# Kernel optimization log

Measured on AMD Instinct MI355X. Metric: run time of the kernel, lower is better.

## Reference

```python
import jax, jax.numpy as jnp
import numpy as np

DIM = 1024
HEADS = 16
HEAD_DIM = DIM // HEADS
LAYERS = 8
HIDDEN = 4 * DIM
VOCAB = 266
MAX_POS = 32768
B = 4
L = 2048
SCALE = HEAD_DIM ** -0.5
EPS = 1e-5


def layer_norm(x, g, b):
    m = jnp.mean(x, axis=-1, keepdims=True)
    v = jnp.mean(jnp.square(x - m), axis=-1, keepdims=True)
    return (x - m) * jax.lax.rsqrt(v + EPS) * g + b


def setup_inputs() -> dict:
    key = jax.random.key(0)
    ks = jax.random.split(key, 16)
    s = 0.02
    return {
        "tokens": jax.random.randint(ks[0], (B, L), 0, VOCAB),
        "tok_emb": jax.random.normal(ks[1], (VOCAB, DIM), jnp.float32) * s,
        "pos_emb": jax.random.normal(ks[2], (MAX_POS, DIM), jnp.float32) * s,
        "ln1_g": jnp.ones((LAYERS, DIM), jnp.float32),
        "ln1_b": jnp.zeros((LAYERS, DIM), jnp.float32),
        "q_w": jax.random.normal(ks[3], (LAYERS, DIM, DIM), jnp.float32) * s,
        "k_w": jax.random.normal(ks[4], (LAYERS, DIM, DIM), jnp.float32) * s,
        "v_w": jax.random.normal(ks[5], (LAYERS, DIM, DIM), jnp.float32) * s,
        "o_w": jax.random.normal(ks[6], (LAYERS, DIM, DIM), jnp.float32) * s,
        "ln2_g": jnp.ones((LAYERS, DIM), jnp.float32),
        "ln2_b": jnp.zeros((LAYERS, DIM), jnp.float32),
        "w1_w": jax.random.normal(ks[7], (LAYERS, HIDDEN, DIM), jnp.float32) * s,
        "wg_w": jax.random.normal(ks[8], (LAYERS, HIDDEN, DIM), jnp.float32) * s,
        "w2_w": jax.random.normal(ks[9], (LAYERS, DIM, HIDDEN), jnp.float32) * s,
        "lnf_g": jnp.ones((DIM,), jnp.float32),
        "lnf_b": jnp.zeros((DIM,), jnp.float32),
        "lm_w": jax.random.normal(ks[10], (VOCAB, DIM), jnp.float32) * s,
    }


def reference(tokens, tok_emb, pos_emb, ln1_g, ln1_b, q_w, k_w, v_w, o_w,
              ln2_g, ln2_b, w1_w, wg_w, w2_w, lnf_g, lnf_b, lm_w):
    Bv, Lv = tokens.shape
    x = tok_emb[tokens] + pos_emb[jnp.arange(Lv)][None, :, :]  # [B,L,D]
    # strictly-upper-triangular causal mask (True = masked)
    rows = jnp.arange(Lv)
    mask = rows[None, :] > rows[:, None]  # [L,L], col > row
    pos_bias = jnp.arange(Lv, dtype=x.dtype) * 0.01  # [L]
    neg_inf = jnp.array(-jnp.inf, dtype=x.dtype)

    for i in range(LAYERS):
        h = layer_norm(x, ln1_g[i], ln1_b[i])
        q = jnp.einsum('bld,ed->ble', h, q_w[i]).reshape(Bv, Lv, HEADS, HEAD_DIM).transpose(0, 2, 1, 3)
        k = jnp.einsum('bld,ed->ble', h, k_w[i]).reshape(Bv, Lv, HEADS, HEAD_DIM).transpose(0, 2, 1, 3)
        v = jnp.einsum('bld,ed->ble', h, v_w[i]).reshape(Bv, Lv, HEADS, HEAD_DIM).transpose(0, 2, 1, 3)
        attn = jnp.einsum('bhqd,bhkd->bhqk', q, k) * SCALE
        attn = jnp.where(mask[None, None, :, :], neg_inf, attn)
        attn = attn + pos_bias[None, None, None, :]
        attn = jax.nn.softmax(attn, axis=-1)
        out = jnp.einsum('bhqk,bhkd->bhqd', attn, v).transpose(0, 2, 1, 3).reshape(Bv, Lv, DIM)
        attn_out = jnp.einsum('bld,ed->ble', out, o_w[i])
        x = x + attn_out
        h2 = layer_norm(x, ln2_g[i], ln2_b[i])
        ff = jnp.einsum('blh,dh->bld', jax.nn.silu(jnp.einsum('bld,hd->blh', h2, w1_w[i])) * jnp.einsum('bld,hd->blh', h2, wg_w[i]), w2_w[i])
        x = x + ff

    last = layer_norm(x[:, -1, :], lnf_g, lnf_b)  # [B, D]
    return jnp.einsum('bd,vd->bv', last, lm_w)  # [B, VOCAB]
```

## Files before the change

kernel.cpp:

```cpp
#include <hip/hip_runtime.h>
#include <hip/hip_bf16.h>
#include <math.h>

#define DIMD 1024
#define HEADS 16
#define HD 64
#define LAYERS 8
#define HIDDEN 4096
#define VOCAB 266
#define NB 4
#define SEQ 2048
#define ROWS (NB*SEQ)
#define LOG2E 1.4426950408889634f
#define QSCALE (0.125f * LOG2E)
#define BIAS2 (0.01f * LOG2E)
#define THR2 8.0f

typedef float f32x4 __attribute__((ext_vector_type(4)));
typedef __bf16 bf16x8 __attribute__((ext_vector_type(8)));
typedef __bf16 bf16x4 __attribute__((ext_vector_type(4)));

__device__ __forceinline__ f32x4 mfma16(bf16x8 a, bf16x8 b, f32x4 c) {
    return __builtin_amdgcn_mfma_f32_16x16x32_bf16(a, b, c, 0, 0, 0);
}

__device__ __forceinline__ void gload16(const __bf16* g, __bf16* l) {
    __builtin_amdgcn_global_load_lds(
        (const __attribute__((address_space(1))) void*)g,
        (__attribute__((address_space(3))) void*)l, 16, 0, 0);
}

__global__ void embed_kernel(const int* __restrict__ tok, const float* __restrict__ te,
                             const float* __restrict__ pe, float* __restrict__ x) {
    int row = blockIdx.x;
    int t = tok[row];
    int l = row & (SEQ - 1);
    int c = threadIdx.x;
    f32x4 tv = *(const f32x4*)(te + (size_t)t * DIMD + c * 4);
    f32x4 pv = *(const f32x4*)(pe + (size_t)l * DIMD + c * 4);
    *(f32x4*)(x + (size_t)row * DIMD + c * 4) = tv + pv;
}

__global__ void cvt_kernel(const float* q, const float* k, const float* v, const float* o,
                           const float* w1, const float* wg, const float* w2,
                           __bf16* __restrict__ dst) {
    const size_t MM = 1024 * 1024;
    const float* src; size_t n; size_t off; int ilv = 0;
    switch (blockIdx.y) {
        case 0: src = q;  n = MM;     off = 0;       break;
        case 1: src = k;  n = MM;     off = MM;      break;
        case 2: src = v;  n = MM;     off = 2 * MM;  break;
        case 3: src = o;  n = MM;     off = 3 * MM;  break;
        case 4: src = w1; n = 4 * MM; off = 4 * MM;  ilv = 1; break;
        case 5: src = wg; n = 4 * MM; off = 4 * MM;  ilv = 2; break;
        default: src = w2; n = 4 * MM; off = 12 * MM; break;
    }
    size_t stride = (size_t)gridDim.x * blockDim.x * 8;
    for (size_t i = ((size_t)blockIdx.x * blockDim.x + threadIdx.x) * 8; i < n; i += stride) {
        f32x4 a = *(const f32x4*)(src + i);
        f32x4 b = *(const f32x4*)(src + i + 4);
        bf16x8 ov;
        ov[0] = (__bf16)a[0]; ov[1] = (__bf16)a[1]; ov[2] = (__bf16)a[2]; ov[3] = (__bf16)a[3];
        ov[4] = (__bf16)b[0]; ov[5] = (__bf16)b[1]; ov[6] = (__bf16)b[2]; ov[7] = (__bf16)b[3];
        size_t di;
        if (ilv) {
            size_t row = i >> 10, col = i & 1023;
            di = off + (((row << 1) | (ilv - 1)) << 10) + col;
        } else {
            di = off + i;
        }
        *(bf16x8*)(dst + di) = ov;
    }
}

template<bool F32OUT>
__global__ void ln_kernel(const float* __restrict__ xin, size_t row_stride,
                          const float* __restrict__ g, const float* __restrict__ bb,
                          void* __restrict__ out) {
    int row = blockIdx.x;
    int c = threadIdx.x;
    const float* xr = xin + (size_t)row * row_stride;
    f32x4 v = *(const f32x4*)(xr + c * 4);
    float s = v[0] + v[1] + v[2] + v[3];
    float s2 = v[0]*v[0] + v[1]*v[1] + v[2]*v[2] + v[3]*v[3];
    #pragma unroll
    for (int o = 32; o; o >>= 1) { s += __shfl_xor(s, o); s2 += __shfl_xor(s2, o); }
    __shared__ float red[8];
    int w = c >> 6, lane = c & 63;
    if (lane == 0) { red[w] = s; red[4 + w] = s2; }
    __syncthreads();
    s = red[0] + red[1] + red[2] + red[3];
    s2 = red[4] + red[5] + red[6] + red[7];
    float mean = s * (1.f / DIMD);
    float var = s2 * (1.f / DIMD) - mean * mean;
    float rstd = rsqrtf(var + 1e-5f);
    f32x4 gv = *(const f32x4*)(g + c * 4);
    f32x4 bv = *(const f32x4*)(bb + c * 4);
    f32x4 o4;
    #pragma unroll
    for (int j = 0; j < 4; ++j) o4[j] = (v[j] - mean) * rstd * gv[j] + bv[j];
    if (F32OUT) {
        *(f32x4*)((float*)out + (size_t)row * DIMD + c * 4) = o4;
    } else {
        bf16x4 hv;
        #pragma unroll
        for (int j = 0; j < 4; ++j) hv[j] = (__bf16)o4[j];
        *(bf16x4*)((__bf16*)out + (size_t)row * DIMD + c * 4) = hv;
    }
}

template<int EPI>
__global__ __launch_bounds__(256, 3)
void gemm_bt(const __bf16* __restrict__ A, const __bf16* __restrict__ W,
             int M, int N, int K,
             __bf16* bdst, float* fdst, float scale) {
    __shared__ __bf16 As[128 * 64];
    __shared__ __bf16 Bs[128 * 64];
    int tid = threadIdx.x;
    int lane = tid & 63, w = tid >> 6;
    int wm = w >> 1, wn = w & 1;
    int g16 = lane >> 4, l16 = lane & 15;
    int m0 = blockIdx.y * 128, n0 = blockIdx.x * 128;
    f32x4 acc[4][4] = {};
    int trow = tid >> 3;
    int cs8 = ((tid & 7) ^ (trow & 7)) * 8;
    const __bf16* ga = A + (size_t)(m0 + trow) * K + cs8;
    const __bf16* gb = W + (size_t)(n0 + trow) * K + cs8;
    int xsw = (l16 & 7) << 4;

    for (int k0 = 0; k0 < K; k0 += 64) {
        #pragma unroll
        for (int p = 0; p < 4; ++p) {
            gload16(ga + (size_t)(p * 32) * K + k0, As + (p * 256 + w * 64) * 8);
            gload16(gb + (size_t)(p * 32) * K + k0, Bs + (p * 256 + w * 64) * 8);
        }
        __syncthreads();
        #pragma unroll
        for (int kk = 0; kk < 2; ++kk) {
            bf16x8 af[4], bfv[4];
            #pragma unroll
            for (int f = 0; f < 4; ++f) {
                int ar = wm * 64 + f * 16 + l16;
                int br = wn * 64 + f * 16 + l16;
                af[f]  = *(const bf16x8*)((const char*)As + ((ar * 128 + kk * 64 + g16 * 16) ^ xsw));
                bfv[f] = *(const bf16x8*)((const char*)Bs + ((br * 128 + kk * 64 + g16 * 16) ^ xsw));
            }
            #pragma unroll
            for (int fm = 0; fm < 4; ++fm)
                #pragma unroll
                for (int fn = 0; fn < 4; ++fn)
                    acc[fm][fn] = mfma16(af[fm], bfv[fn], acc[fm][fn]);
        }
        __syncthreads();
    }

    #pragma unroll
    for (int fm = 0; fm < 4; ++fm) {
        int rbase = m0 + wm * 64 + fm * 16 + g16 * 4;
        #pragma unroll
        for (int fn = 0; fn < 4; ++fn) {
            int col = n0 + wn * 64 + fn * 16 + l16;
            if (EPI == 2) {
                #pragma unroll
                for (int j = 0; j < 4; ++j) {
                    size_t idx = (size_t)(rbase + j) * N + col;
                    fdst[idx] += acc[fm][fn][j];
                }
            }
        }
    }
}

template<int EPI>
__global__ __launch_bounds__(512, 2)
void gemm_8ph(const __bf16* __restrict__ A, const __bf16* __restrict__ W,
              int M, int N, int K, __bf16* __restrict__ bdst, float scale) {
    __shared__ __bf16 As[2][2][128 * 64];
    __shared__ __bf16 Bs[2][2][128 * 64];
    int tid = threadIdx.x;
    int lane = tid & 63, wid = tid >> 6;
    int wm = wid >> 2, wn = wid & 3;
    int g16 = lane >> 4, l16 = lane & 15;
    int m0 = blockIdx.y * 256, n0 = blockIdx.x * 256;

    int sr = tid >> 3, ch = tid & 7;
    int cs8 = (ch ^ (sr & 7)) * 8;
    int xsw = (l16 & 7) << 4;

    const __bf16* gA = A + (size_t)(m0 + sr) * K + cs8;
    const __bf16* gB = W + (size_t)(n0 + sr) * K + cs8;

    auto stA = [&](int buf, int half, int kt) {
        const __bf16* g = gA + (size_t)(half * 128) * K + kt * 64;
        __bf16* l = &As[buf][half][sr * 64 + ch * 8];
        gload16(g, l);
        gload16(g + (size_t)64 * K, l + 64 * 64);
    };
    auto stB = [&](int buf, int half, int kt) {
        const __bf16* g = gB + (size_t)(half * 128) * K + kt * 64;
        __bf16* l = &Bs[buf][half][sr * 64 + ch * 8];
        gload16(g, l);
        gload16(g + (size_t)64 * K, l + 64 * 64);
    };

    f32x4 acc[8][4] = {};
    bf16x8 bfr[4][2];

    auto dsA = [&](int buf, int q, bf16x8 (&afr)[2][2]) {
        const char* base = (const char*)&As[buf][wm][0];
        #pragma unroll
        for (int dm = 0; dm < 2; ++dm)
            #pragma unroll
            for (int kk = 0; kk < 2; ++kk) {
                int row = (q * 2 + dm) * 16 + l16;
                afr[dm][kk] = *(const bf16x8*)(base + ((row * 128 + kk * 64 + g16 * 16) ^ xsw));
            }
    };
    auto dsB = [&](int buf) {
        const char* base = (const char*)&Bs[buf][wn >> 1][0];
        #pragma unroll
        for (int n = 0; n < 4; ++n)
            #pragma unroll
            for (int kk = 0; kk < 2; ++kk) {
                int row = (wn & 1) * 64 + n * 16 + l16;
                bfr[n][kk] = *(const bf16x8*)(base + ((row * 128 + kk * 64 + g16 * 16) ^ xsw));
            }
    };
    auto mm = [&](int q, bf16x8 (&afr)[2][2]) {
        #pragma unroll
        for (int dm = 0; dm < 2; ++dm)
            #pragma unroll
            for (int n = 0; n < 4; ++n)
                #pragma unroll
                for (int kk = 0; kk < 2; ++kk)
                    acc[q * 2 + dm][n] = mfma16(afr[dm][kk], bfr[n][kk], acc[q * 2 + dm][n]);
    };

#define PH(Q)                                                \
    __builtin_amdgcn_s_barrier();                            \
    asm volatile("s_waitcnt lgkmcnt(0)" ::: "memory");       \
    __builtin_amdgcn_s_setprio(1);                           \
    mm(Q, afr);                                              \
    __builtin_amdgcn_s_setprio(0);

    int NI = K >> 7;

    stA(0, 0, 0); stA(0, 1, 0); stB(0, 0, 0); stB(0, 1, 0);
    stB(1, 0, 1); stB(1, 1, 1);
    asm volatile("s_waitcnt vmcnt(4)" ::: "memory");
    __builtin_amdgcn_s_barrier();

    for (int it = 0; it < NI; ++it) {
        bool more = (it + 1 < NI);
        int o = 2 * it + 1, e2 = o + 1, o2 = o + 2;
        { bf16x8 afr[2][2]; dsA(0, 0, afr); dsB(0); stA(1, 0, o);    PH(0); }
        { bf16x8 afr[2][2]; dsA(0, 1, afr); stA(1, 1, o);            PH(1); }
        { bf16x8 afr[2][2]; dsA(0, 2, afr); if (more) stB(0, 0, e2); PH(2); }
        { bf16x8 afr[2][2]; dsA(0, 3, afr); if (more) stB(0, 1, e2);
          if (more) asm volatile("s_waitcnt vmcnt(4)" ::: "memory");
          else      asm volatile("s_waitcnt vmcnt(0)" ::: "memory");
          PH(3); }
        { bf16x8 afr[2][2]; dsA(1, 0, afr); dsB(1); if (more) stA(0, 0, e2); PH(0); }
        { bf16x8 afr[2][2]; dsA(1, 1, afr); if (more) stA(0, 1, e2); PH(1); }
        { bf16x8 afr[2][2]; dsA(1, 2, afr); if (more) stB(1, 0, o2); PH(2); }
        { bf16x8 afr[2][2]; dsA(1, 3, afr); if (more) stB(1, 1, o2);
          if (more) asm volatile("s_waitcnt vmcnt(4)" ::: "memory");
          PH(3); }
    }
#undef PH

    #pragma unroll
    for (int m = 0; m < 8; ++m) {
        int rbase = m0 + wm * 128 + m * 16 + g16 * 4;
        #pragma unroll
        for (int n = 0; n < 4; ++n) {
            int col = n0 + wn * 64 + n * 16 + l16;
            if (EPI == 5) {
                int which = col >> 10;
                int c = col & 1023;
                int hh = c >> 6, d = c & 63;
                if (which == 2) {
                    int b = rbase >> 11, l = rbase & 2047;
                    __bf16* vp = bdst + 2 * (size_t)ROWS * DIMD;
                    bf16x4 hv;
                    #pragma unroll
                    for (int j = 0; j < 4; ++j) hv[j] = (__bf16)acc[m][n][j];
                    *(bf16x4*)(vp + ((size_t)(b * HEADS + hh) * HD + d) * SEQ + l) = hv;
                } else {
                    float sc = (which == 0) ? scale : 1.f;
                    __bf16* base = bdst + (size_t)which * ROWS * DIMD;
                    #pragma unroll
                    for (int j = 0; j < 4; ++j) {
                        int row = rbase + j;
                        int b = row >> 11, l = row & 2047;
                        base[(((size_t)(b * HEADS + hh) * SEQ + l) << 6) + d] =
                            (__bf16)(acc[m][n][j] * sc);
                    }
                }
            } else if (EPI == 6) {
                #pragma unroll
                for (int j = 0; j < 4; ++j) {
                    float own = acc[m][n][j];
                    float other = __shfl_xor(own, 1);
                    if (!(l16 & 1)) {
                        float si = own / (1.f + __expf(-own));
                        bdst[(size_t)(rbase + j) * (N >> 1) + (col >> 1)] = (__bf16)(si * other);
                    }
                }
            }
        }
    }
}

__global__ __launch_bounds__(256, 2)
void attn_kernel(const __bf16* __restrict__ qt, const __bf16* __restrict__ kt,
                 const __bf16* __restrict__ vt, __bf16* __restrict__ ao) {
    int lin = blockIdx.x;
    int bxm = lin >> 6;
    int g = lin & 63;
    int hh = g & 15, b = g >> 4;
    int tid = threadIdx.x, lane = tid & 63, w = tid >> 6;
    int g16 = lane >> 4, l16 = lane & 15;

    __shared__ __bf16 Ks[2][64 * 64];
    __shared__ __bf16 Vs[2][64 * 64];
    __shared__ __bf16 Ps[4 * 32 * 72];
    __bf16* Pw = Ps + w * (32 * 72);

    const __bf16* qbase = qt + (size_t)(b * HEADS + hh) * SEQ * HD;
    const __bf16* kbase = kt + (size_t)(b * HEADS + hh) * SEQ * HD;
    const __bf16* vbase = vt + (size_t)(b * HEADS + hh) * HD * SEQ;

    int rr = lane >> 3;
    int cs8 = ((lane & 7) ^ rr) * 8;

    for (int s = 0; s < 2; ++s) {
        int qtile = (s == 0) ? (15 - bxm) : bxm;
        int qb = qtile * 128;
        int nt = (qb >> 6) + 2;

        bf16x8 qf[2][2];
        #pragma unroll
        for (int rb = 0; rb < 2; ++rb)
            #pragma unroll
            for (int kk = 0; kk < 2; ++kk)
                qf[rb][kk] = *(const bf16x8*)(qbase + (size_t)(qb + w * 32 + rb * 16 + l16) * HD + kk * 32 + g16 * 8);

        f32x4 accO[2][4] = {};
        float mrow[2][4], lrow[2][4];
        #pragma unroll
        for (int rb = 0; rb < 2; ++rb)
            #pragma unroll
            for (int j = 0; j < 4; ++j) { mrow[rb][j] = -1e30f; lrow[rb][j] = 0.f; }

        #pragma unroll
        for (int p = 0; p < 2; ++p) {
            int rbse = p * 32 + w * 8;
            gload16(kbase + (size_t)(rbse + rr) * HD + cs8, Ks[0] + rbse * 64);
            gload16(vbase + (size_t)(rbse + rr) * SEQ + cs8, Vs[0] + rbse * 64);
        }
        __syncthreads();

        for (int t = 0; t < nt; ++t) {
            int cur = t & 1;
            int kv0 = t << 6;

            if (t + 1 < nt) {
                int kv1 = kv0 + 64;
                #pragma unroll
                for (int p = 0; p < 2; ++p) {
                    int rbse = p * 32 + w * 8;
                    gload16(kbase + (size_t)(kv1 + rbse + rr) * HD + cs8, Ks[cur ^ 1] + rbse * 64);
                    gload16(vbase + (size_t)(rbse + rr) * SEQ + kv1 + cs8, Vs[cur ^ 1] + rbse * 64);
                }
            }

            f32x4 sacc[2][4] = {};
            __builtin_amdgcn_s_setprio(1);
            #pragma unroll
            for (int kk = 0; kk < 2; ++kk) {
                bf16x8 kf[4];
                #pragma unroll
                for (int nk = 0; nk < 4; ++nk) {
                    int key = nk * 16 + l16;
                    int bo = (key * 128 + (kk * 32 + g16 * 8) * 2) ^ ((key & 7) << 4);
                    kf[nk] = *(const bf16x8*)((const char*)Ks[cur] + bo);
                }
                #pragma unroll
                for (int rb = 0; rb < 2; ++rb)
                    #pragma unroll
                    for (int nk = 0; nk < 4; ++nk)
                        sacc[rb][nk] = mfma16(qf[rb][kk], kf[nk], sacc[rb][nk]);
            }
            __builtin_amdgcn_s_setprio(0);

            float mx8[2][4];
            #pragma unroll
            for (int rb = 0; rb < 2; ++rb) {
                #pragma unroll
                for (int j = 0; j < 4; ++j) {
                    int qrow = qb + w * 32 + rb * 16 + g16 * 4 + j;
                    float mx = -1e30f;
                    #pragma unroll
                    for (int nk = 0; nk < 4; ++nk) {
                        int key = kv0 + nk * 16 + l16;
                        float sc = sacc[rb][nk][j];
                        sc = (key <= qrow) ? (sc + BIAS2 * (float)key) : -1e30f;
                        sacc[rb][nk][j] = sc;
                        mx = fmaxf(mx, sc);
                    }
                    mx = fmaxf(mx, __shfl_xor(mx, 1));
                    mx = fmaxf(mx, __shfl_xor(mx, 2));
                    mx = fmaxf(mx, __shfl_xor(mx, 4));
                    mx = fmaxf(mx, __shfl_xor(mx, 8));
                    mx8[rb][j] = mx;
                }
            }

            bool ok = true;
            #pragma unroll
            for (int rb = 0; rb < 2; ++rb)
                #pragma unroll
                for (int j = 0; j < 4; ++j)
                    ok &= (mx8[rb][j] <= mrow[rb][j] + THR2);
            if (!__all(ok)) {
                #pragma unroll
                for (int rb = 0; rb < 2; ++rb) {
                    #pragma unroll
                    for (int j = 0; j < 4; ++j) {
                        float mnew = fmaxf(mrow[rb][j], mx8[rb][j]);
                        float rs = exp2f(mrow[rb][j] - mnew);
                        mrow[rb][j] = mnew;
                        lrow[rb][j] *= rs;
                        #pragma unroll
                        for (int nd = 0; nd < 4; ++nd) accO[rb][nd][j] *= rs;
                    }
                }
            }

            #pragma unroll
            for (int rb = 0; rb < 2; ++rb) {
                #pragma unroll
                for (int j = 0; j < 4; ++j) {
                    float m = mrow[rb][j];
                    float ps = 0.f;
                    #pragma unroll
                    for (int nk = 0; nk < 4; ++nk) {
                        float pp = exp2f(sacc[rb][nk][j] - m);
                        ps += pp;
                        Pw[(rb * 16 + g16 * 4 + j) * 72 + nk * 16 + l16] = (__bf16)pp;
                    }
                    lrow[rb][j] += ps;
                }
            }

            __builtin_amdgcn_s_setprio(1);
            #pragma unroll
            for (int kk = 0; kk < 2; ++kk) {
                bf16x8 pf[2];
                #pragma unroll
                for (int rb = 0; rb < 2; ++rb)
                    pf[rb] = *(const bf16x8*)(Pw + (rb * 16 + l16) * 72 + kk * 32 + g16 * 8);
                #pragma unroll
                for (int nd = 0; nd < 4; ++nd) {
                    int d = nd * 16 + l16;
                    int bo = (d * 128 + (kk * 32 + g16 * 8) * 2) ^ ((d & 7) << 4);
                    bf16x8 vf = *(const bf16x8*)((const char*)Vs[cur] + bo);
                    #pragma unroll
                    for (int rb = 0; rb < 2; ++rb)
                        accO[rb][nd] = mfma16(pf[rb], vf, accO[rb][nd]);
                }
            }
            __builtin_amdgcn_s_setprio(0);
            __syncthreads();
        }

        #pragma unroll
        for (int rb = 0; rb < 2; ++rb) {
            #pragma unroll
            for (int j = 0; j < 4; ++j) {
                float l = lrow[rb][j];
                l += __shfl_xor(l, 1);
                l += __shfl_xor(l, 2);
                l += __shfl_xor(l, 4);
                l += __shfl_xor(l, 8);
                lrow[rb][j] = 1.f / l;
            }
        }
        #pragma unroll
        for (int rb = 0; rb < 2; ++rb)
            #pragma unroll
            for (int nd = 0; nd < 4; ++nd)
                #pragma unroll
                for (int j = 0; j < 4; ++j) {
                    int row = qb + w * 32 + rb * 16 + g16 * 4 + j;
                    float o = accO[rb][nd][j] * lrow[rb][j];
                    ao[(size_t)(b * SEQ + row) * DIMD + hh * HD + nd * 16 + l16] = (__bf16)o;
                }
    }
}

__global__ void lm_head(const float* __restrict__ last, const float* __restrict__ lw,
                        float* __restrict__ out) {
    int v = blockIdx.x;
    int c = threadIdx.x, lane = c & 63, w = c >> 6;
    f32x4 wv = *(const f32x4*)(lw + (size_t)v * DIMD + c * 4);
    float a[NB];
    #pragma unroll
    for (int b = 0; b < NB; ++b) {
        f32x4 xv = *(const f32x4*)(last + b * DIMD + c * 4);
        a[b] = wv[0]*xv[0] + wv[1]*xv[1] + wv[2]*xv[2] + wv[3]*xv[3];
    }
    #pragma unroll
    for (int o = 32; o; o >>= 1)
        #pragma unroll
        for (int b = 0; b < NB; ++b) a[b] += __shfl_xor(a[b], o);
    __shared__ float red[4][NB];
    if (lane == 0)
        #pragma unroll
        for (int b = 0; b < NB; ++b) red[w][b] = a[b];
    __syncthreads();
    if (c < NB) {
        float s = red[0][c] + red[1][c] + red[2][c] + red[3][c];
        out[c * VOCAB + v] = s;
    }
}

extern "C" void kernel_launch(void* const* d_in, const int* in_sizes, int n_in,
                              void* d_out, int out_size, void* d_ws, size_t ws_size,
                              hipStream_t stream) {
    const int*   tokens  = (const int*)d_in[0];
    const float* tok_emb = (const float*)d_in[1];
    const float* pos_emb = (const float*)d_in[2];
    const float* ln1_g   = (const float*)d_in[3];
    const float* ln1_b   = (const float*)d_in[4];
    const float* q_w     = (const float*)d_in[5];
    const float* k_w     = (const float*)d_in[6];
    const float* v_w     = (const float*)d_in[7];
    const float* o_w     = (const float*)d_in[8];
    const float* ln2_g   = (const float*)d_in[9];
    const float* ln2_b   = (const float*)d_in[10];
    const float* w1_w    = (const float*)d_in[11];
    const float* wg_w    = (const float*)d_in[12];
    const float* w2_w    = (const float*)d_in[13];
    const float* lnf_g   = (const float*)d_in[14];
    const float* lnf_b   = (const float*)d_in[15];
    const float* lm_w    = (const float*)d_in[16];

    const size_t MM = 1024 * 1024;
    char* p = (char*)d_ws;
    __bf16* wbf = (__bf16*)p;          p += 16 * MM * 2;
    float*  x   = (float*)p;           p += (size_t)ROWS * DIMD * 4;
    __bf16* h   = (__bf16*)p;          p += (size_t)ROWS * DIMD * 2;
    __bf16* qt  = (__bf16*)p;          p += (size_t)ROWS * DIMD * 2;
    __bf16* kt  = (__bf16*)p;          p += (size_t)ROWS * DIMD * 2;
    __bf16* vt  = (__bf16*)p;          p += (size_t)ROWS * DIMD * 2;
    __bf16* ao  = (__bf16*)p;          p += (size_t)ROWS * DIMD * 2;
    __bf16* abuf= (__bf16*)p;          p += (size_t)ROWS * HIDDEN * 2;
    float*  last= (float*)p;           p += NB * DIMD * 4;

    embed_kernel<<<ROWS, 256, 0, stream>>>(tokens, tok_emb, pos_emb, x);

    for (int i = 0; i < LAYERS; ++i) {
        cvt_kernel<<<dim3(256, 7), 256, 0, stream>>>(
            q_w + (size_t)i * MM, k_w + (size_t)i * MM, v_w + (size_t)i * MM, o_w + (size_t)i * MM,
            w1_w + (size_t)i * 4 * MM, wg_w + (size_t)i * 4 * MM, w2_w + (size_t)i * 4 * MM, wbf);
        __bf16* wqkv = wbf;
        __bf16* wo   = wbf + 3 * MM;
        __bf16* w1g  = wbf + 4 * MM;
        __bf16* w2   = wbf + 12 * MM;

        ln_kernel<false><<<ROWS, 256, 0, stream>>>(x, DIMD, ln1_g + i * DIMD, ln1_b + i * DIMD, h);

        gemm_8ph<5><<<dim3(12, 32), 512, 0, stream>>>(h, wqkv, ROWS, 3 * DIMD, DIMD, qt, QSCALE);

        attn_kernel<<<512, 256, 0, stream>>>(qt, kt, vt, ao);

        gemm_bt<2><<<dim3(8, 64), 256, 0, stream>>>(ao, wo, ROWS, DIMD, DIMD, nullptr, x, 1.f);

        ln_kernel<false><<<ROWS, 256, 0, stream>>>(x, DIMD, ln2_g + i * DIMD, ln2_b + i * DIMD, h);

        gemm_8ph<6><<<dim3(32, 32), 512, 0, stream>>>(h, w1g, ROWS, 2 * HIDDEN, DIMD, abuf, 1.f);

        gemm_bt<2><<<dim3(8, 64), 256, 0, stream>>>(abuf, w2, ROWS, DIMD, HIDDEN, nullptr, x, 1.f);
    }

    ln_kernel<true><<<NB, 256, 0, stream>>>(x + (size_t)(SEQ - 1) * DIMD, (size_t)SEQ * DIMD,
                                            lnf_g, lnf_b, last);
    lm_head<<<VOCAB, 256, 0, stream>>>(last, lm_w, (float*)d_out);
}
```

Measured before the change: 4.053 ms.

## Split attention q-tiles into separate blocks and move FFN up-projection to 128-tile GEMM

The attention kernel now launches 1024 blocks, one q-tile each, instead of 512 blocks that each processed a heavy and a light tile in sequence. Occupancy hints are raised for attention (3) and gemm_bt (4). The SwiGLU up-projection moves from the 256x256 8-phase GEMM to the 128x128 gemm_bt with a new EPI==6 epilogue, and an unused EPI==5 path is added to gemm_bt. The aim is more parallelism and better load balance, at the cost of losing the paired-tile balancing in attention and the larger tile reuse in the FFN GEMM.

```diff
diff --git a/kernel.cpp b/kernel.cpp
--- a/kernel.cpp
+++ b/kernel.cpp
@@ -110,7 +110,7 @@
 }
 
 template<int EPI>
-__global__ __launch_bounds__(256, 3)
+__global__ __launch_bounds__(256, 4)
 void gemm_bt(const __bf16* __restrict__ A, const __bf16* __restrict__ W,
              int M, int N, int K,
              __bf16* bdst, float* fdst, float scale) {
@@ -165,6 +165,38 @@
                 for (int j = 0; j < 4; ++j) {
                     size_t idx = (size_t)(rbase + j) * N + col;
                     fdst[idx] += acc[fm][fn][j];
+                }
+            } else if (EPI == 5) {
+                int which = col >> 10;
+                int c = col & 1023;
+                int hh = c >> 6, d = c & 63;
+                if (which == 2) {
+                    int b = rbase >> 11, l = rbase & 2047;
+                    __bf16* vp = bdst + 2 * (size_t)ROWS * DIMD;
+                    bf16x4 hv;
+                    #pragma unroll
+                    for (int j = 0; j < 4; ++j) hv[j] = (__bf16)acc[fm][fn][j];
+                    *(bf16x4*)(vp + ((size_t)(b * HEADS + hh) * HD + d) * SEQ + l) = hv;
+                } else {
+                    float sc = (which == 0) ? scale : 1.f;
+                    __bf16* base = bdst + (size_t)which * ROWS * DIMD;
+                    #pragma unroll
+                    for (int j = 0; j < 4; ++j) {
+                        int row = rbase + j;
+                        int b = row >> 11, l = row & 2047;
+                        base[(((size_t)(b * HEADS + hh) * SEQ + l) << 6) + d] =
+                            (__bf16)(acc[fm][fn][j] * sc);
+                    }
+                }
+            } else if (EPI == 6) {
+                #pragma unroll
+                for (int j = 0; j < 4; ++j) {
+                    float own = acc[fm][fn][j];
+                    float other = __shfl_xor(own, 1);
+                    if (!(l16 & 1)) {
+                        float si = own / (1.f + __expf(-own));
+                        bdst[(size_t)(rbase + j) * (N >> 1) + (col >> 1)] = (__bf16)(si * other);
+                    }
                 }
             }
         }
@@ -297,27 +329,16 @@
                             (__bf16)(acc[m][n][j] * sc);
                     }
                 }
-            } else if (EPI == 6) {
-                #pragma unroll
-                for (int j = 0; j < 4; ++j) {
-                    float own = acc[m][n][j];
-                    float other = __shfl_xor(own, 1);
-                    if (!(l16 & 1)) {
-                        float si = own / (1.f + __expf(-own));
-                        bdst[(size_t)(rbase + j) * (N >> 1) + (col >> 1)] = (__bf16)(si * other);
-                    }
-                }
-            }
-        }
-    }
-}
-
-__global__ __launch_bounds__(256, 2)
+            }
+        }
+    }
+}
+
+__global__ __launch_bounds__(256, 3)
 void attn_kernel(const __bf16* __restrict__ qt, const __bf16* __restrict__ kt,
                  const __bf16* __restrict__ vt, __bf16* __restrict__ ao) {
-    int lin = blockIdx.x;
-    int bxm = lin >> 6;
-    int g = lin & 63;
+    int qtile = 15 - (blockIdx.x >> 6);
+    int g = blockIdx.x & 63;
     int hh = g & 15, b = g >> 4;
     int tid = threadIdx.x, lane = tid & 63, w = tid >> 6;
     int g16 = lane >> 4, l16 = lane & 15;
@@ -334,170 +355,167 @@
     int rr = lane >> 3;
     int cs8 = ((lane & 7) ^ rr) * 8;
 
-    for (int s = 0; s < 2; ++s) {
-        int qtile = (s == 0) ? (15 - bxm) : bxm;
-        int qb = qtile * 128;
-        int nt = (qb >> 6) + 2;
-
-        bf16x8 qf[2][2];
+    int qb = qtile * 128;
+    int nt = (qb >> 6) + 2;
+
+    bf16x8 qf[2][2];
+    #pragma unroll
+    for (int rb = 0; rb < 2; ++rb)
+        #pragma unroll
+        for (int kk = 0; kk < 2; ++kk)
+            qf[rb][kk] = *(const bf16x8*)(qbase + (size_t)(qb + w * 32 + rb * 16 + l16) * HD + kk * 32 + g16 * 8);
+
+    f32x4 accO[2][4] = {};
+    float mrow[2][4], lrow[2][4];
+    #pragma unroll
+    for (int rb = 0; rb < 2; ++rb)
+        #pragma unroll
+        for (int j = 0; j < 4; ++j) { mrow[rb][j] = -1e30f; lrow[rb][j] = 0.f; }
+
+    #pragma unroll
+    for (int p = 0; p < 2; ++p) {
+        int rbse = p * 32 + w * 8;
+        gload16(kbase + (size_t)(rbse + rr) * HD + cs8, Ks[0] + rbse * 64);
+        gload16(vbase + (size_t)(rbse + rr) * SEQ + cs8, Vs[0] + rbse * 64);
+    }
+    __syncthreads();
+
+    for (int t = 0; t < nt; ++t) {
+        int cur = t & 1;
+        int kv0 = t << 6;
+
+        if (t + 1 < nt) {
+            int kv1 = kv0 + 64;
+            #pragma unroll
+            for (int p = 0; p < 2; ++p) {
+                int rbse = p * 32 + w * 8;
+                gload16(kbase + (size_t)(kv1 + rbse + rr) * HD + cs8, Ks[cur ^ 1] + rbse * 64);
+                gload16(vbase + (size_t)(rbse + rr) * SEQ + kv1 + cs8, Vs[cur ^ 1] + rbse * 64);
+            }
+        }
+
+        f32x4 sacc[2][4] = {};
+        __builtin_amdgcn_s_setprio(1);
+        #pragma unroll
+        for (int kk = 0; kk < 2; ++kk) {
+            bf16x8 kf[4];
+            #pragma unroll
+            for (int nk = 0; nk < 4; ++nk) {
+                int key = nk * 16 + l16;
+                int bo = (key * 128 + (kk * 32 + g16 * 8) * 2) ^ ((key & 7) << 4);
+                kf[nk] = *(const bf16x8*)((const char*)Ks[cur] + bo);
+            }
+            #pragma unroll
+            for (int rb = 0; rb < 2; ++rb)
+                #pragma unroll
+                for (int nk = 0; nk < 4; ++nk)
+                    sacc[rb][nk] = mfma16(qf[rb][kk], kf[nk], sacc[rb][nk]);
+        }
+        __builtin_amdgcn_s_setprio(0);
+
+        float mx8[2][4];
+        #pragma unroll
+        for (int rb = 0; rb < 2; ++rb) {
+            #pragma unroll
+            for (int j = 0; j < 4; ++j) {
+                int qrow = qb + w * 32 + rb * 16 + g16 * 4 + j;
+                float mx = -1e30f;
+                #pragma unroll
+                for (int nk = 0; nk < 4; ++nk) {
+                    int key = kv0 + nk * 16 + l16;
+                    float sc = sacc[rb][nk][j];
+                    sc = (key <= qrow) ? (sc + BIAS2 * (float)key) : -1e30f;
+                    sacc[rb][nk][j] = sc;
+                    mx = fmaxf(mx, sc);
+                }
+                mx = fmaxf(mx, __shfl_xor(mx, 1));
+                mx = fmaxf(mx, __shfl_xor(mx, 2));
+                mx = fmaxf(mx, __shfl_xor(mx, 4));
+                mx = fmaxf(mx, __shfl_xor(mx, 8));
+                mx8[rb][j] = mx;
+            }
+        }
+
+        bool ok = true;
         #pragma unroll
         for (int rb = 0; rb < 2; ++rb)
             #pragma unroll
-            for (int kk = 0; kk < 2; ++kk)
-                qf[rb][kk] = *(const bf16x8*)(qbase + (size_t)(qb + w * 32 + rb * 16 + l16) * HD + kk * 32 + g16 * 8);
-
-        f32x4 accO[2][4] = {};
-        float mrow[2][4], lrow[2][4];
-        #pragma unroll
-        for (int rb = 0; rb < 2; ++rb)
-            #pragma unroll
-            for (int j = 0; j < 4; ++j) { mrow[rb][j] = -1e30f; lrow[rb][j] = 0.f; }
-
-        #pragma unroll
-        for (int p = 0; p < 2; ++p) {
-            int rbse = p * 32 + w * 8;
-            gload16(kbase + (size_t)(rbse + rr) * HD + cs8, Ks[0] + rbse * 64);
-            gload16(vbase + (size_t)(rbse + rr) * SEQ + cs8, Vs[0] + rbse * 64);
-        }
+            for (int j = 0; j < 4; ++j)
+                ok &= (mx8[rb][j] <= mrow[rb][j] + THR2);
+        if (!__all(ok)) {
+            #pragma unroll
+            for (int rb = 0; rb < 2; ++rb) {
+                #pragma unroll
+                for (int j = 0; j < 4; ++j) {
+                    float mnew = fmaxf(mrow[rb][j], mx8[rb][j]);
+                    float rs = exp2f(mrow[rb][j] - mnew);
+                    mrow[rb][j] = mnew;
+                    lrow[rb][j] *= rs;
+                    #pragma unroll
+                    for (int nd = 0; nd < 4; ++nd) accO[rb][nd][j] *= rs;
+                }
+            }
+        }
+
+        #pragma unroll
+        for (int rb = 0; rb < 2; ++rb) {
+            #pragma unroll
+            for (int j = 0; j < 4; ++j) {
+                float m = mrow[rb][j];
+                float ps = 0.f;
+                #pragma unroll
+                for (int nk = 0; nk < 4; ++nk) {
+                    float pp = exp2f(sacc[rb][nk][j] - m);
+                    ps += pp;
+                    Pw[(rb * 16 + g16 * 4 + j) * 72 + nk * 16 + l16] = (__bf16)pp;
+                }
+                lrow[rb][j] += ps;
+            }
+        }
+
+        __builtin_amdgcn_s_setprio(1);
+        #pragma unroll
+        for (int kk = 0; kk < 2; ++kk) {
+            bf16x8 pf[2];
+            #pragma unroll
+            for (int rb = 0; rb < 2; ++rb)
+                pf[rb] = *(const bf16x8*)(Pw + (rb * 16 + l16) * 72 + kk * 32 + g16 * 8);
+            #pragma unroll
+            for (int nd = 0; nd < 4; ++nd) {
+                int d = nd * 16 + l16;
+                int bo = (d * 128 + (kk * 32 + g16 * 8) * 2) ^ ((d & 7) << 4);
+                bf16x8 vf = *(const bf16x8*)((const char*)Vs[cur] + bo);
+                #pragma unroll
+                for (int rb = 0; rb < 2; ++rb)
+                    accO[rb][nd] = mfma16(pf[rb], vf, accO[rb][nd]);
+            }
+        }
+        __builtin_amdgcn_s_setprio(0);
         __syncthreads();
-
-        for (int t = 0; t < nt; ++t) {
-            int cur = t & 1;
-            int kv0 = t << 6;
-
-            if (t + 1 < nt) {
-                int kv1 = kv0 + 64;
-                #pragma unroll
-                for (int p = 0; p < 2; ++p) {
-                    int rbse = p * 32 + w * 8;
-                    gload16(kbase + (size_t)(kv1 + rbse + rr) * HD + cs8, Ks[cur ^ 1] + rbse * 64);
-                    gload16(vbase + (size_t)(rbse + rr) * SEQ + kv1 + cs8, Vs[cur ^ 1] + rbse * 64);
-                }
-            }
-
-            f32x4 sacc[2][4] = {};
-            __builtin_amdgcn_s_setprio(1);
-            #pragma unroll
-            for (int kk = 0; kk < 2; ++kk) {
-                bf16x8 kf[4];
-                #pragma unroll
-                for (int nk = 0; nk < 4; ++nk) {
-                    int key = nk * 16 + l16;
-                    int bo = (key * 128 + (kk * 32 + g16 * 8) * 2) ^ ((key & 7) << 4);
-                    kf[nk] = *(const bf16x8*)((const char*)Ks[cur] + bo);
-                }
-                #pragma unroll
-                for (int rb = 0; rb < 2; ++rb)
-                    #pragma unroll
-                    for (int nk = 0; nk < 4; ++nk)
-                        sacc[rb][nk] = mfma16(qf[rb][kk], kf[nk], sacc[rb][nk]);
-            }
-            __builtin_amdgcn_s_setprio(0);
-
-            float mx8[2][4];
-            #pragma unroll
-            for (int rb = 0; rb < 2; ++rb) {
-                #pragma unroll
-                for (int j = 0; j < 4; ++j) {
-                    int qrow = qb + w * 32 + rb * 16 + g16 * 4 + j;
-                    float mx = -1e30f;
-                    #pragma unroll
-                    for (int nk = 0; nk < 4; ++nk) {
-                        int key = kv0 + nk * 16 + l16;
-                        float sc = sacc[rb][nk][j];
-                        sc = (key <= qrow) ? (sc + BIAS2 * (float)key) : -1e30f;
-                        sacc[rb][nk][j] = sc;
-                        mx = fmaxf(mx, sc);
-                    }
-                    mx = fmaxf(mx, __shfl_xor(mx, 1));
-                    mx = fmaxf(mx, __shfl_xor(mx, 2));
-                    mx = fmaxf(mx, __shfl_xor(mx, 4));
-                    mx = fmaxf(mx, __shfl_xor(mx, 8));
-                    mx8[rb][j] = mx;
-                }
-            }
-
-            bool ok = true;
-            #pragma unroll
-            for (int rb = 0; rb < 2; ++rb)
-                #pragma unroll
-                for (int j = 0; j < 4; ++j)
-                    ok &= (mx8[rb][j] <= mrow[rb][j] + THR2);
-            if (!__all(ok)) {
-                #pragma unroll
-                for (int rb = 0; rb < 2; ++rb) {
-                    #pragma unroll
-                    for (int j = 0; j < 4; ++j) {
-                        float mnew = fmaxf(mrow[rb][j], mx8[rb][j]);
-                        float rs = exp2f(mrow[rb][j] - mnew);
-                        mrow[rb][j] = mnew;
-                        lrow[rb][j] *= rs;
-                        #pragma unroll
-                        for (int nd = 0; nd < 4; ++nd) accO[rb][nd][j] *= rs;
-                    }
-                }
-            }
-
-            #pragma unroll
-            for (int rb = 0; rb < 2; ++rb) {
-                #pragma unroll
-                for (int j = 0; j < 4; ++j) {
-                    float m = mrow[rb][j];
-                    float ps = 0.f;
-                    #pragma unroll
-                    for (int nk = 0; nk < 4; ++nk) {
-                        float pp = exp2f(sacc[rb][nk][j] - m);
-                        ps += pp;
-                        Pw[(rb * 16 + g16 * 4 + j) * 72 + nk * 16 + l16] = (__bf16)pp;
-                    }
-                    lrow[rb][j] += ps;
-                }
-            }
-
-            __builtin_amdgcn_s_setprio(1);
-            #pragma unroll
-            for (int kk = 0; kk < 2; ++kk) {
-                bf16x8 pf[2];
-                #pragma unroll
-                for (int rb = 0; rb < 2; ++rb)
-                    pf[rb] = *(const bf16x8*)(Pw + (rb * 16 + l16) * 72 + kk * 32 + g16 * 8);
-                #pragma unroll
-                for (int nd = 0; nd < 4; ++nd) {
-                    int d = nd * 16 + l16;
-                    int bo = (d * 128 + (kk * 32 + g16 * 8) * 2) ^ ((d & 7) << 4);
-                    bf16x8 vf = *(const bf16x8*)((const char*)Vs[cur] + bo);
-                    #pragma unroll
-                    for (int rb = 0; rb < 2; ++rb)
-                        accO[rb][nd] = mfma16(pf[rb], vf, accO[rb][nd]);
-                }
-            }
-            __builtin_amdgcn_s_setprio(0);
-            __syncthreads();
-        }
-
-        #pragma unroll
-        for (int rb = 0; rb < 2; ++rb) {
+    }
+
+    #pragma unroll
+    for (int rb = 0; rb < 2; ++rb) {
+        #pragma unroll
+        for (int j = 0; j < 4; ++j) {
+            float l = lrow[rb][j];
+            l += __shfl_xor(l, 1);
+            l += __shfl_xor(l, 2);
+            l += __shfl_xor(l, 4);
+            l += __shfl_xor(l, 8);
+            lrow[rb][j] = 1.f / l;
+        }
+    }
+    #pragma unroll
+    for (int rb = 0; rb < 2; ++rb)
+        #pragma unroll
+        for (int nd = 0; nd < 4; ++nd)
             #pragma unroll
             for (int j = 0; j < 4; ++j) {
-                float l = lrow[rb][j];
-                l += __shfl_xor(l, 1);
-                l += __shfl_xor(l, 2);
-                l += __shfl_xor(l, 4);
-                l += __shfl_xor(l, 8);
-                lrow[rb][j] = 1.f / l;
-            }
-        }
-        #pragma unroll
-        for (int rb = 0; rb < 2; ++rb)
-            #pragma unroll
-            for (int nd = 0; nd < 4; ++nd)
-                #pragma unroll
-                for (int j = 0; j < 4; ++j) {
-                    int row = qb + w * 32 + rb * 16 + g16 * 4 + j;
-                    float o = accO[rb][nd][j] * lrow[rb][j];
-                    ao[(size_t)(b * SEQ + row) * DIMD + hh * HD + nd * 16 + l16] = (__bf16)o;
-                }
-    }
+                int row = qb + w * 32 + rb * 16 + g16 * 4 + j;
+                float o = accO[rb][nd][j] * lrow[rb][j];
+                ao[(size_t)(b * SEQ + row) * DIMD + hh * HD + nd * 16 + l16] = (__bf16)o;
+            }
 }
 
 __global__ void lm_head(const float* __restrict__ last, const float* __restrict__ lw,
@@ -574,13 +592,13 @@
 
         gemm_8ph<5><<<dim3(12, 32), 512, 0, stream>>>(h, wqkv, ROWS, 3 * DIMD, DIMD, qt, QSCALE);
 
-        attn_kernel<<<512, 256, 0, stream>>>(qt, kt, vt, ao);
+        attn_kernel<<<1024, 256, 0, stream>>>(qt, kt, vt, ao);
 
         gemm_bt<2><<<dim3(8, 64), 256, 0, stream>>>(ao, wo, ROWS, DIMD, DIMD, nullptr, x, 1.f);
 
         ln_kernel<false><<<ROWS, 256, 0, stream>>>(x, DIMD, ln2_g + i * DIMD, ln2_b + i * DIMD, h);
 
-        gemm_8ph<6><<<dim3(32, 32), 512, 0, stream>>>(h, w1g, ROWS, 2 * HIDDEN, DIMD, abuf, 1.f);
+        gemm_bt<6><<<dim3(64, 64), 256, 0, stream>>>(h, w1g, ROWS, 2 * HIDDEN, DIMD, abuf, nullptr, 1.f);
 
         gemm_bt<2><<<dim3(8, 64), 256, 0, stream>>>(abuf, w2, ROWS, DIMD, HIDDEN, nullptr, x, 1.f);
     }
```

Measured after the change: 3.819 ms. -5.8%, faster.
